# Performance work log

Measured on AMD Instinct MI355X. Metric: run time of the kernel, lower is better.

The kernel has to match this reference:

```python
import jax, jax.numpy as jnp
import numpy as np

D = 1024
H = 16
HD = D // H
T = 2048
B = 2
EPS = 1e-6


def rmsnorm(x, w):
    xf = x.astype(jnp.float32)
    n = xf * jax.lax.rsqrt(jnp.mean(xf * xf, axis=-1, keepdims=True) + EPS)
    return n.astype(x.dtype) * w


def setup_inputs() -> dict:
    key = jax.random.key(0)
    ks = jax.random.split(key, 12)
    s_in = 1.0 / np.sqrt(D)
    s_h = 1.0 / np.sqrt(HD * H)
    s_ff = 1.0 / np.sqrt(4 * D)
    return {
        "x": jax.random.normal(ks[0], (B, T, D), jnp.float32),
        "wq": jax.random.normal(ks[1], (H, D, HD), jnp.float32) * s_in,
        "wk": jax.random.normal(ks[2], (H, D, HD), jnp.float32) * s_in,
        "wv": jax.random.normal(ks[3], (H, D, HD), jnp.float32) * s_in,
        "w_proj": jax.random.normal(ks[4], (D, D), jnp.float32) * s_h,
        "b_proj": jax.random.normal(ks[5], (D,), jnp.float32) * 0.01,
        "w1": jax.random.normal(ks[6], (D, 8 * D), jnp.float32) * s_in,
        "b1": jax.random.normal(ks[7], (8 * D,), jnp.float32) * 0.01,
        "w2": jax.random.normal(ks[8], (4 * D, D), jnp.float32) * s_ff,
        "b2": jax.random.normal(ks[9], (D,), jnp.float32) * 0.01,
        "g1": jnp.ones((D,), jnp.float32),
        "g2": jnp.ones((D,), jnp.float32),
    }


def reference(x, wq, wk, wv, w_proj, b_proj, w1, b1, w2, b2, g1, g2):
    # --- attention sub-block ---
    xn = rmsnorm(x, g1)
    q = jnp.einsum("btd,hde->bhte", xn, wq)  # [B,H,T,HD]
    k = jnp.einsum("btd,hde->bhte", xn, wk)
    v = jnp.einsum("btd,hde->bhte", xn, wv)
    scores = jnp.einsum("bhte,bhse->bhts", q, k) * (HD ** -0.5)
    causal = jnp.tril(jnp.ones((T, T), bool))
    scores = jnp.where(causal, scores, -jnp.inf)
    attn = jax.nn.softmax(scores, axis=-1)
    o = jnp.einsum("bhts,bhse->bhte", attn, v)  # [B,H,T,HD]
    o = o.transpose(0, 2, 1, 3).reshape(B, T, H * HD)  # concat heads
    x = x + o @ w_proj + b_proj
    # --- GLU FFN sub-block ---
    xn2 = rmsnorm(x, g2)
    h = xn2 @ w1 + b1  # [B,T,8D]
    a, b = jnp.split(h, 2, axis=-1)
    glu = a * jax.nn.sigmoid(b)  # [B,T,4D]
    x = x + glu @ w2 + b2
    return x
```

## Files before the change

### kernel.cpp

```cpp
#include <hip/hip_runtime.h>


typedef __attribute__((ext_vector_type(4))) float f32x4;
typedef __attribute__((ext_vector_type(8))) short short8;

typedef __attribute__((address_space(1))) const void gvoid;
typedef __attribute__((address_space(3))) void lvoid;

static __device__ __forceinline__ void gl_lds16(const void* g, void* l) {
  __builtin_amdgcn_global_load_lds((gvoid*)g, (lvoid*)l, 16, 0, 0);
}

static __device__ __forceinline__ unsigned short f2bf(float f) {
  union { float f; unsigned u; } v; v.f = f;
  unsigned r = v.u + 0x7fffu + ((v.u >> 16) & 1u);
  return (unsigned short)(r >> 16);
}
static __device__ __forceinline__ float to_f32(float v) { return v; }
static __device__ __forceinline__ float to_f32(unsigned short v) {
  union { unsigned u; float f; } x; x.u = ((unsigned)v) << 16; return x.f;
}

static __device__ __forceinline__ f32x4 mfma16(short8 a, short8 b, f32x4 c) {
  return __builtin_amdgcn_mfma_f32_16x16x32_bf16(a, b, c, 0, 0, 0);
}

template <typename Tin>
__global__ __launch_bounds__(256) void transpose_cvt(
    const Tin* __restrict__ in, unsigned short* __restrict__ out,
    int in_ld, long in_bstride, int out_ld, long out_bstride)
{
  __shared__ float tile[64][65];
  const Tin* inp = in + (long)blockIdx.z * in_bstride;
  unsigned short* outp = out + (long)blockIdx.z * out_bstride;
  int r0 = blockIdx.y * 64, c0 = blockIdx.x * 64;
  int tx = threadIdx.x & 63, ty = threadIdx.x >> 6;
#pragma unroll
  for (int i = ty; i < 64; i += 4)
    tile[i][tx] = to_f32(inp[(long)(r0 + i) * in_ld + (c0 + tx)]);
  __syncthreads();
#pragma unroll
  for (int i = ty; i < 64; i += 4)
    outp[(long)(c0 + i) * out_ld + (r0 + tx)] = f2bf(tile[tx][i]);
}

__global__ __launch_bounds__(256) void rmsnorm_k(
    const float* __restrict__ x, const float* __restrict__ g,
    unsigned short* __restrict__ out)
{
  int row = blockIdx.x;
  int t = threadIdx.x;
  float4 v = ((const float4*)(x + (long)row * 1024))[t];
  float ss = v.x * v.x + v.y * v.y + v.z * v.z + v.w * v.w;
#pragma unroll
  for (int ofs = 32; ofs; ofs >>= 1) ss += __shfl_down(ss, ofs);
  __shared__ float red[4];
  if ((t & 63) == 0) red[t >> 6] = ss;
  __syncthreads();
  float sc = rsqrtf((red[0] + red[1] + red[2] + red[3]) * (1.0f / 1024.0f) + 1e-6f);
  float4 gv = ((const float4*)g)[t];
  ushort4 o4;
  o4.x = f2bf(v.x * sc * gv.x); o4.y = f2bf(v.y * sc * gv.y);
  o4.z = f2bf(v.z * sc * gv.z); o4.w = f2bf(v.w * sc * gv.w);
  ((ushort4*)(out + (long)row * 1024))[t] = o4;
}

template <int EPI, int WM_, int WN_, bool GLUB>
__global__ __launch_bounds__(256, 2) void gemm_bt(
    const unsigned short* __restrict__ A, const unsigned short* __restrict__ Bt,
    unsigned short* __restrict__ outb, float* __restrict__ outf,
    const float* __restrict__ res, const float* __restrict__ bias,
    int K, int lda, int ldbt, int ldout)
{
  constexpr int FM = 128 / (16 * WM_);
  constexpr int FN = 128 / (16 * WN_);
  __shared__ alignas(16) unsigned short Asm_[2 * 128 * 64];
  __shared__ alignas(16) unsigned short Bsm_[2 * 128 * 64];
  const int tid = threadIdx.x, lane = tid & 63, wave = tid >> 6;
  const int lr = lane & 15, lg = lane >> 4;
  const int wr = wave / WN_, wc = wave % WN_;
  const int m0 = blockIdx.y * 128;

  f32x4 acc[FM][FN];
#pragma unroll
  for (int mi = 0; mi < FM; mi++)
#pragma unroll
    for (int ni = 0; ni < FN; ni++) acc[mi][ni] = f32x4{0.f, 0.f, 0.f, 0.f};

  int arow[4], au[4];
  long brow[4];
#pragma unroll
  for (int i = 0; i < 4; i++) {
    int U = tid + 256 * i;
    arow[i] = U >> 3;
    au[i] = ((U & 7) ^ (arow[i] & 7)) * 8;
    if (GLUB)
      brow[i] = (arow[i] < 64) ? (long)(blockIdx.x * 64 + arow[i])
                               : (long)(4096 + blockIdx.x * 64 + arow[i] - 64);
    else
      brow[i] = (long)blockIdx.x * 128 + arow[i];
  }

  auto stage = [&](int buf, int k0) {
#pragma unroll
    for (int i = 0; i < 4; i++) {
      gl_lds16(A + (long)(m0 + arow[i]) * lda + k0 + au[i],
               (char*)Asm_ + (buf * 1024 + wave * 64 + 256 * i) * 16);
      gl_lds16(Bt + brow[i] * ldbt + k0 + au[i],
               (char*)Bsm_ + (buf * 1024 + wave * 64 + 256 * i) * 16);
    }
  };

  stage(0, 0);
  if (K > 64) stage(1, 64);

  int it = 0;
  for (int k0 = 0; k0 < K; k0 += 64, it++) {
    if (k0 + 64 < K) asm volatile("s_waitcnt vmcnt(8)" ::: "memory");
    else             asm volatile("s_waitcnt vmcnt(0)" ::: "memory");
    __builtin_amdgcn_s_barrier();

    const int cur = it & 1;
    const char* ab = (const char*)Asm_ + cur * 16384;
    const char* bb = (const char*)Bsm_ + cur * 16384;

    short8 af[FM][2], bfr[FN][2];
#pragma unroll
    for (int mi = 0; mi < FM; mi++) {
      int row = wr * 16 * FM + mi * 16 + lr;
#pragma unroll
      for (int kk = 0; kk < 2; kk++) {
        int off = row * 128 + (((kk * 4 + lg) ^ (row & 7)) & 7) * 16;
        af[mi][kk] = *(const short8*)(ab + off);
      }
    }
#pragma unroll
    for (int ni = 0; ni < FN; ni++) {
      int row = wc * 16 * FN + ni * 16 + lr;
#pragma unroll
      for (int kk = 0; kk < 2; kk++) {
        int off = row * 128 + (((kk * 4 + lg) ^ (row & 7)) & 7) * 16;
        bfr[ni][kk] = *(const short8*)(bb + off);
      }
    }
    __builtin_amdgcn_s_setprio(1);
#pragma unroll
    for (int kk = 0; kk < 2; kk++)
#pragma unroll
      for (int mi = 0; mi < FM; mi++)
#pragma unroll
        for (int ni = 0; ni < FN; ni++)
          acc[mi][ni] = mfma16(af[mi][kk], bfr[ni][kk], acc[mi][ni]);
    __builtin_amdgcn_s_setprio(0);

    __builtin_amdgcn_s_barrier();
    if (k0 + 128 < K) stage(cur, k0 + 128);
  }

  const int rb = m0 + wr * 16 * FM + 4 * lg;
  if constexpr (EPI == 0) {
#pragma unroll
    for (int mi = 0; mi < FM; mi++)
#pragma unroll
      for (int ni = 0; ni < FN; ni++) {
        int col = blockIdx.x * 128 + wc * 16 * FN + ni * 16 + lr;
#pragma unroll
        for (int r = 0; r < 4; r++)
          outb[(long)(rb + mi * 16 + r) * ldout + col] = f2bf(acc[mi][ni][r]);
      }
  } else if constexpr (EPI == 1) {
#pragma unroll
    for (int mi = 0; mi < FM; mi++)
#pragma unroll
      for (int ni = 0; ni < FN; ni++) {
        int col = blockIdx.x * 128 + wc * 16 * FN + ni * 16 + lr;
        float bv = bias[col];
#pragma unroll
        for (int r = 0; r < 4; r++) {
          long idx = (long)(rb + mi * 16 + r) * ldout + col;
          outf[idx] = acc[mi][ni][r] + res[idx] + bv;
        }
      }
  } else {
#pragma unroll
    for (int mi = 0; mi < FM; mi++)
#pragma unroll
      for (int ni = 0; ni < FN / 2; ni++) {
        int col = blockIdx.x * 64 + ni * 16 + lr;
        float ba = bias[col], bb2 = bias[4096 + col];
#pragma unroll
        for (int r = 0; r < 4; r++) {
          float a = acc[mi][ni][r] + ba;
          float b = acc[mi][ni + FN / 2][r] + bb2;
          float s = 1.0f / (1.0f + __expf(-b));
          outb[(long)(rb + mi * 16 + r) * ldout + col] = f2bf(a * s);
        }
      }
  }
}

__global__ __launch_bounds__(256, 2) void attn_k(
    const unsigned short* __restrict__ qkv, const unsigned short* __restrict__ vt,
    unsigned short* __restrict__ o)
{
  __shared__ alignas(16) unsigned short Ksm[2 * 128 * 64];
  __shared__ alignas(16) unsigned short Vsm[2 * 64 * 128];
  __shared__ alignas(16) unsigned short Psm[4][16 * 128];
  const int tid = threadIdx.x, lane = tid & 63, wave = tid >> 6;
  const int lr = lane & 15, lg = lane >> 4;
  const int bh = blockIdx.y, b = bh >> 4, h = bh & 15;
  const int ia = blockIdx.x;
  const int tA0 = ia * 64, tB0 = (31 - ia) * 64;
  const int nchA = (ia + 2) >> 1, nchB = (33 - ia) >> 1;
  const float NEGINF = -__builtin_inff();

  short8 qfA[2], qfB[2];
  {
    const unsigned short* qp =
        qkv + (long)(b * 2048 + tA0 + wave * 16 + lr) * 3072 + h * 64 + lg * 8;
    qfA[0] = *(const short8*)qp;  qfA[1] = *(const short8*)(qp + 32);
    qp = qkv + (long)(b * 2048 + tB0 + wave * 16 + lr) * 3072 + h * 64 + lg * 8;
    qfB[0] = *(const short8*)qp;  qfB[1] = *(const short8*)(qp + 32);
  }
  f32x4 oA[4], oB[4];
#pragma unroll
  for (int n = 0; n < 4; n++) { oA[n] = f32x4{0,0,0,0}; oB[n] = f32x4{0,0,0,0}; }
  float mA = NEGINF, lA = 0.f, mB = NEGINF, lB = 0.f;

  const long kbase = (long)(b * 2048) * 3072 + 1024 + h * 64;
  const long vbase = (long)bh * 64 * 2048;

  auto stage = [&](int buf, int c) {
    const int s0 = c * 128;
#pragma unroll
    for (int i = 0; i < 4; i++) {
      int U = tid + 256 * i;
      int kr = U >> 3, ku = (U ^ kr) & 7;
      gl_lds16(qkv + kbase + (long)(s0 + kr) * 3072 + ku * 8,
               (char*)Ksm + (buf * 1024 + wave * 64 + 256 * i) * 16);
      int vr = U >> 4, vu = (U & 8) | ((U ^ vr) & 7);
      gl_lds16(vt + vbase + (long)vr * 2048 + s0 + vu * 8,
               (char*)Vsm + (buf * 1024 + wave * 64 + 256 * i) * 16);
    }
  };

  char* pb = (char*)&Psm[wave][0];

  auto process = [&](const short8* qf, f32x4* o_acc, float& m, float& l,
                     const char* kb, const char* vb, int s0, int qg, bool diag) {
    f32x4 s[8];
#pragma unroll
    for (int n = 0; n < 8; n++) s[n] = f32x4{0.f, 0.f, 0.f, 0.f};
    __builtin_amdgcn_s_setprio(1);
#pragma unroll
    for (int n = 0; n < 8; n++) {
      int row = n * 16 + lr;
#pragma unroll
      for (int kk = 0; kk < 2; kk++) {
        int off = row * 128 + (((kk * 4 + lg) ^ row) & 7) * 16;
        short8 kf = *(const short8*)(kb + off);
        s[n] = mfma16(kf, qf[kk], s[n]);
      }
    }
    __builtin_amdgcn_s_setprio(0);
#pragma unroll
    for (int n = 0; n < 8; n++)
#pragma unroll
      for (int r = 0; r < 4; r++) {
        float v = s[n][r] * 0.125f;
        if (diag && (s0 + n * 16 + 4 * lg + r > qg)) v = NEGINF;
        s[n][r] = v;
      }
    float t[8];
#pragma unroll
    for (int n = 0; n < 8; n++)
      t[n] = fmaxf(fmaxf(s[n][0], s[n][1]), fmaxf(s[n][2], s[n][3]));
    float mx = fmaxf(fmaxf(fmaxf(t[0], t[1]), fmaxf(t[2], t[3])),
                     fmaxf(fmaxf(t[4], t[5]), fmaxf(t[6], t[7])));
    mx = fmaxf(mx, __shfl_xor(mx, 16));
    mx = fmaxf(mx, __shfl_xor(mx, 32));
    if (!__all(mx <= m + 8.0f)) {
      float mn = fmaxf(m, mx);
      float alpha = __expf(m - mn);
      m = mn;
      l *= alpha;
#pragma unroll
      for (int r = 0; r < 4; r++) {
        float ar = __shfl(alpha, 4 * lg + r);
#pragma unroll
        for (int n = 0; n < 4; n++) o_acc[n][r] *= ar;
      }
    }
    float sum = 0.f;
#pragma unroll
    for (int n = 0; n < 8; n++)
#pragma unroll
      for (int r = 0; r < 4; r++) {
        float p = __expf(s[n][r] - m);
        s[n][r] = p;
        sum += p;
      }
    sum += __shfl_xor(sum, 16);
    sum += __shfl_xor(sum, 32);
    l += sum;
#pragma unroll
    for (int n = 0; n < 8; n++) {
      unsigned lo = (unsigned)f2bf(s[n][0]) | ((unsigned)f2bf(s[n][1]) << 16);
      unsigned hi = (unsigned)f2bf(s[n][2]) | ((unsigned)f2bf(s[n][3]) << 16);
      int u = 2 * n + (lg >> 1);
      int su = (u & 8) | ((u ^ lr) & 7);
      *(uint2*)(pb + lr * 256 + su * 16 + 8 * (lg & 1)) = uint2{lo, hi};
    }
    asm volatile("s_waitcnt lgkmcnt(0)" ::: "memory");
    __builtin_amdgcn_sched_barrier(0);
    short8 pa[4];
#pragma unroll
    for (int ks = 0; ks < 4; ks++) {
      int u = 4 * ks + lg;
      int su = (u & 8) | ((u ^ lr) & 7);
      pa[ks] = *(const short8*)(pb + lr * 256 + su * 16);
    }
    __builtin_amdgcn_s_setprio(1);
#pragma unroll
    for (int n = 0; n < 4; n++) {
      int row = n * 16 + lr;
#pragma unroll
      for (int ks = 0; ks < 4; ks++) {
        int u = 4 * ks + lg;
        int su = (u & 8) | ((u ^ row) & 7);
        short8 vf = *(const short8*)(vb + row * 256 + su * 16);
        o_acc[n] = mfma16(pa[ks], vf, o_acc[n]);
      }
    }
    __builtin_amdgcn_s_setprio(0);
  };

  stage(0, 0);
  __syncthreads();

  const int qgA = tA0 + wave * 16 + lr, qgB = tB0 + wave * 16 + lr;
  for (int c = 0; c < nchB; c++) {
    if (c + 1 < nchB) stage((c + 1) & 1, c + 1);
    const char* kb = (const char*)Ksm + (c & 1) * 16384;
    const char* vb = (const char*)Vsm + (c & 1) * 16384;
    const int s0 = c * 128;
    if (c < nchA) process(qfA, oA, mA, lA, kb, vb, s0, qgA, c == nchA - 1);
    process(qfB, oB, mB, lB, kb, vb, s0, qgB, c == nchB - 1);
    __syncthreads();
  }

  auto finish = [&](const f32x4* o_acc, float l, int t0) {
#pragma unroll
    for (int r = 0; r < 4; r++) {
      float inv = 1.0f / __shfl(l, 4 * lg + r);
      int trow = t0 + wave * 16 + 4 * lg + r;
#pragma unroll
      for (int n = 0; n < 4; n++)
        o[(long)(b * 2048 + trow) * 1024 + h * 64 + n * 16 + lr] =
            f2bf(o_acc[n][r] * inv);
    }
  };
  finish(oA, lA, tA0);
  finish(oB, lB, tB0);
}

extern "C" void kernel_launch(void* const* d_in, const int* in_sizes, int n_in,
                              void* d_out, int out_size, void* d_ws, size_t ws_size,
                              hipStream_t stream) {
  const float* x     = (const float*)d_in[0];
  const float* wq    = (const float*)d_in[1];
  const float* wk    = (const float*)d_in[2];
  const float* wv    = (const float*)d_in[3];
  const float* wproj = (const float*)d_in[4];
  const float* bproj = (const float*)d_in[5];
  const float* w1    = (const float*)d_in[6];
  const float* b1    = (const float*)d_in[7];
  const float* w2    = (const float*)d_in[8];
  const float* b2    = (const float*)d_in[9];
  const float* g1    = (const float*)d_in[10];
  const float* g2    = (const float*)d_in[11];
  (void)in_sizes; (void)n_in; (void)out_size; (void)ws_size;

  char* ws = (char*)d_ws;
  unsigned short* wt_qkv = (unsigned short*)(ws);
  unsigned short* wpt    = (unsigned short*)(ws + (6ul << 20));
  unsigned short* w1t    = (unsigned short*)(ws + (8ul << 20));
  unsigned short* w2t    = (unsigned short*)(ws + (24ul << 20));
  unsigned short* xn     = (unsigned short*)(ws + (32ul << 20));
  unsigned short* qkv    = (unsigned short*)(ws + (40ul << 20));
  unsigned short* vt     = (unsigned short*)(ws + (64ul << 20));
  unsigned short* glu    = (unsigned short*)(ws + (40ul << 20));
  unsigned short* obuf   = (unsigned short*)(ws + (72ul << 20));
  float*          x1     = (float*)(ws + (80ul << 20));
  float* outf = (float*)d_out;

  transpose_cvt<float><<<dim3(1, 16, 16), 256, 0, stream>>>(
      wq, wt_qkv, 64, (long)1024 * 64, 1024, (long)64 * 1024);
  transpose_cvt<float><<<dim3(1, 16, 16), 256, 0, stream>>>(
      wk, wt_qkv + 1024ul * 1024, 64, (long)1024 * 64, 1024, (long)64 * 1024);
  transpose_cvt<float><<<dim3(1, 16, 16), 256, 0, stream>>>(
      wv, wt_qkv + 2048ul * 1024, 64, (long)1024 * 64, 1024, (long)64 * 1024);
  transpose_cvt<float><<<dim3(16, 16, 1), 256, 0, stream>>>(
      wproj, wpt, 1024, 0, 1024, 0);
  transpose_cvt<float><<<dim3(128, 16, 1), 256, 0, stream>>>(
      w1, w1t, 8192, 0, 1024, 0);
  transpose_cvt<float><<<dim3(16, 64, 1), 256, 0, stream>>>(
      w2, w2t, 1024, 0, 4096, 0);

  rmsnorm_k<<<4096, 256, 0, stream>>>(x, g1, xn);

  gemm_bt<0, 2, 2, false><<<dim3(24, 32), 256, 0, stream>>>(
      xn, wt_qkv, qkv, nullptr, nullptr, nullptr, 1024, 1024, 1024, 3072);

  transpose_cvt<unsigned short><<<dim3(1, 32, 16), 256, 0, stream>>>(
      qkv + 2048, vt, 3072, 64, 2048, (long)64 * 2048);
  transpose_cvt<unsigned short><<<dim3(1, 32, 16), 256, 0, stream>>>(
      qkv + 2048ul * 3072 + 2048, vt + 16ul * 64 * 2048, 3072, 64, 2048, (long)64 * 2048);

  attn_k<<<dim3(16, 32), 256, 0, stream>>>(qkv, vt, obuf);

  gemm_bt<1, 2, 2, false><<<dim3(8, 32), 256, 0, stream>>>(
      obuf, wpt, nullptr, x1, x, bproj, 1024, 1024, 1024, 1024);

  rmsnorm_k<<<4096, 256, 0, stream>>>(x1, g2, xn);

  gemm_bt<2, 4, 1, true><<<dim3(64, 32), 256, 0, stream>>>(
      xn, w1t, glu, nullptr, nullptr, b1, 1024, 1024, 1024, 4096);

  gemm_bt<1, 2, 2, false><<<dim3(8, 32), 256, 0, stream>>>(
      glu, w2t, nullptr, outf, x1, b2, 4096, 4096, 4096, 1024);
}
```

Measured before the change: 313.3 us.

## Drop GEMM double buffering and use 64-row tiles for N=1024 GEMMs

Replaces the double-buffered async LDS pipeline in the bf16 GEMM with a single-buffered load-sync-compute loop, which halves LDS use. A BM template parameter is added, and the two output-projection GEMMs (N=1024) now use 64-row tiles so they launch twice as many blocks and fill more CUs. The trade-off is that loads no longer overlap with MFMA work, so every k-step stalls on global memory latency. The smaller LDS footprint and larger grid are meant to raise occupancy enough to hide that latency instead.

```diff
diff --git a/kernel.cpp b/kernel.cpp
--- a/kernel.cpp
+++ b/kernel.cpp
@@ -65,21 +65,22 @@
   ((ushort4*)(out + (long)row * 1024))[t] = o4;
 }
 
-template <int EPI, int WM_, int WN_, bool GLUB>
+template <int EPI, int BM, int WM_, int WN_, bool GLUB>
 __global__ __launch_bounds__(256, 2) void gemm_bt(
     const unsigned short* __restrict__ A, const unsigned short* __restrict__ Bt,
     unsigned short* __restrict__ outb, float* __restrict__ outf,
     const float* __restrict__ res, const float* __restrict__ bias,
     int K, int lda, int ldbt, int ldout)
 {
-  constexpr int FM = 128 / (16 * WM_);
+  constexpr int FM = BM / (16 * WM_);
   constexpr int FN = 128 / (16 * WN_);
-  __shared__ alignas(16) unsigned short Asm_[2 * 128 * 64];
-  __shared__ alignas(16) unsigned short Bsm_[2 * 128 * 64];
+  constexpr int AR = BM / 32;
+  __shared__ alignas(16) unsigned short Asm_[BM * 64];
+  __shared__ alignas(16) unsigned short Bsm_[128 * 64];
   const int tid = threadIdx.x, lane = tid & 63, wave = tid >> 6;
   const int lr = lane & 15, lg = lane >> 4;
   const int wr = wave / WN_, wc = wave % WN_;
-  const int m0 = blockIdx.y * 128;
+  const int m0 = blockIdx.y * BM;
 
   f32x4 acc[FM][FN];
 #pragma unroll
@@ -87,42 +88,37 @@
 #pragma unroll
     for (int ni = 0; ni < FN; ni++) acc[mi][ni] = f32x4{0.f, 0.f, 0.f, 0.f};
 
-  int arow[4], au[4];
+  int br_[4], bu_[4];
   long brow[4];
 #pragma unroll
   for (int i = 0; i < 4; i++) {
     int U = tid + 256 * i;
-    arow[i] = U >> 3;
-    au[i] = ((U & 7) ^ (arow[i] & 7)) * 8;
+    br_[i] = U >> 3;
+    bu_[i] = ((U & 7) ^ (br_[i] & 7)) * 8;
     if (GLUB)
-      brow[i] = (arow[i] < 64) ? (long)(blockIdx.x * 64 + arow[i])
-                               : (long)(4096 + blockIdx.x * 64 + arow[i] - 64);
+      brow[i] = (br_[i] < 64) ? (long)(blockIdx.x * 64 + br_[i])
+                              : (long)(4096 + blockIdx.x * 64 + br_[i] - 64);
     else
-      brow[i] = (long)blockIdx.x * 128 + arow[i];
-  }
-
-  auto stage = [&](int buf, int k0) {
-#pragma unroll
-    for (int i = 0; i < 4; i++) {
-      gl_lds16(A + (long)(m0 + arow[i]) * lda + k0 + au[i],
-               (char*)Asm_ + (buf * 1024 + wave * 64 + 256 * i) * 16);
-      gl_lds16(Bt + brow[i] * ldbt + k0 + au[i],
-               (char*)Bsm_ + (buf * 1024 + wave * 64 + 256 * i) * 16);
-    }
-  };
-
-  stage(0, 0);
-  if (K > 64) stage(1, 64);
-
-  int it = 0;
-  for (int k0 = 0; k0 < K; k0 += 64, it++) {
-    if (k0 + 64 < K) asm volatile("s_waitcnt vmcnt(8)" ::: "memory");
-    else             asm volatile("s_waitcnt vmcnt(0)" ::: "memory");
-    __builtin_amdgcn_s_barrier();
-
-    const int cur = it & 1;
-    const char* ab = (const char*)Asm_ + cur * 16384;
-    const char* bb = (const char*)Bsm_ + cur * 16384;
+      brow[i] = (long)blockIdx.x * 128 + br_[i];
+  }
+  int ar_[AR], au_[AR];
+#pragma unroll
+  for (int i = 0; i < AR; i++) {
+    int U = tid + 256 * i;
+    ar_[i] = U >> 3;
+    au_[i] = ((U & 7) ^ (ar_[i] & 7)) * 8;
+  }
+
+  for (int k0 = 0; k0 < K; k0 += 64) {
+#pragma unroll
+    for (int i = 0; i < 4; i++)
+      gl_lds16(Bt + brow[i] * ldbt + k0 + bu_[i],
+               (char*)Bsm_ + (wave * 64 + 256 * i) * 16);
+#pragma unroll
+    for (int i = 0; i < AR; i++)
+      gl_lds16(A + (long)(m0 + ar_[i]) * lda + k0 + au_[i],
+               (char*)Asm_ + (wave * 64 + 256 * i) * 16);
+    __syncthreads();
 
     short8 af[FM][2], bfr[FN][2];
 #pragma unroll
@@ -131,7 +127,7 @@
 #pragma unroll
       for (int kk = 0; kk < 2; kk++) {
         int off = row * 128 + (((kk * 4 + lg) ^ (row & 7)) & 7) * 16;
-        af[mi][kk] = *(const short8*)(ab + off);
+        af[mi][kk] = *(const short8*)((const char*)Asm_ + off);
       }
     }
 #pragma unroll
@@ -140,7 +136,7 @@
 #pragma unroll
       for (int kk = 0; kk < 2; kk++) {
         int off = row * 128 + (((kk * 4 + lg) ^ (row & 7)) & 7) * 16;
-        bfr[ni][kk] = *(const short8*)(bb + off);
+        bfr[ni][kk] = *(const short8*)((const char*)Bsm_ + off);
       }
     }
     __builtin_amdgcn_s_setprio(1);
@@ -152,9 +148,7 @@
         for (int ni = 0; ni < FN; ni++)
           acc[mi][ni] = mfma16(af[mi][kk], bfr[ni][kk], acc[mi][ni]);
     __builtin_amdgcn_s_setprio(0);
-
-    __builtin_amdgcn_s_barrier();
-    if (k0 + 128 < K) stage(cur, k0 + 128);
+    __syncthreads();
   }
 
   const int rb = m0 + wr * 16 * FM + 4 * lg;
@@ -409,7 +403,7 @@
 
   rmsnorm_k<<<4096, 256, 0, stream>>>(x, g1, xn);
 
-  gemm_bt<0, 2, 2, false><<<dim3(24, 32), 256, 0, stream>>>(
+  gemm_bt<0, 128, 2, 2, false><<<dim3(24, 32), 256, 0, stream>>>(
       xn, wt_qkv, qkv, nullptr, nullptr, nullptr, 1024, 1024, 1024, 3072);
 
   transpose_cvt<unsigned short><<<dim3(1, 32, 16), 256, 0, stream>>>(
@@ -419,14 +413,14 @@
 
   attn_k<<<dim3(16, 32), 256, 0, stream>>>(qkv, vt, obuf);
 
-  gemm_bt<1, 2, 2, false><<<dim3(8, 32), 256, 0, stream>>>(
+  gemm_bt<1, 64, 2, 2, false><<<dim3(8, 64), 256, 0, stream>>>(
       obuf, wpt, nullptr, x1, x, bproj, 1024, 1024, 1024, 1024);
 
   rmsnorm_k<<<4096, 256, 0, stream>>>(x1, g2, xn);
 
-  gemm_bt<2, 4, 1, true><<<dim3(64, 32), 256, 0, stream>>>(
+  gemm_bt<2, 128, 4, 1, true><<<dim3(64, 32), 256, 0, stream>>>(
       xn, w1t, glu, nullptr, nullptr, b1, 1024, 1024, 1024, 4096);
 
-  gemm_bt<1, 2, 2, false><<<dim3(8, 32), 256, 0, stream>>>(
+  gemm_bt<1, 64, 2, 2, false><<<dim3(8, 64), 256, 0, stream>>>(
       glu, w2t, nullptr, outf, x1, b2, 4096, 4096, 4096, 1024);
 }
```

Measured after the change: 304.5 us. -2.8%, faster.
